# Kernel optimization log

Hardware: AMD Instinct MI355X
Metric: run time of the kernel (lower is better)

The kernel has to match this reference:

```python
import jax, jax.numpy as jnp
import numpy as np

B, S, H = 4, 2048, 1024

def setup_inputs() -> dict:
    key = jax.random.key(0)
    ks = jax.random.split(key, 4)
    scale = 1.0 / np.sqrt(H)
    x = jax.random.normal(ks[0], (B, S, H), dtype=jnp.float32)
    Wq = jax.random.normal(ks[1], (H, H), dtype=jnp.float32) * scale
    Wk = jax.random.normal(ks[2], (H, H), dtype=jnp.float32) * scale
    Wv = jax.random.normal(ks[3], (H, H), dtype=jnp.float32) * scale
    bq = jnp.zeros((H,), dtype=jnp.float32)
    bk = jnp.zeros((H,), dtype=jnp.float32)
    bv = jnp.zeros((H,), dtype=jnp.float32)
    return {"x": x, "Wq": Wq, "bq": bq, "Wk": Wk, "bk": bk, "Wv": Wv, "bv": bv}

def reference(x, Wq, bq, Wk, bk, Wv, bv):
    # Linear: y = x @ W^T + b (torch nn.Linear convention)
    Q = jnp.einsum('bsh,oh->bso', x, Wq) + bq
    K = jnp.einsum('bsh,oh->bso', x, Wk) + bk
    V = jnp.einsum('bsh,oh->bso', x, Wv) + bv
    scores = jnp.einsum('bqh,bkh->bqk', Q, K) / jnp.sqrt(jnp.float32(H))
    attn = jax.nn.softmax(scores, axis=-1)
    return jnp.einsum('bqk,bkh->bqh', attn, V)
```

## Files before the change

kernel.cpp:

```cpp
#include <hip/hip_runtime.h>
#include <cstdint>
#include <cstddef>


typedef __bf16 bf16;
typedef _Float16 f16;
typedef __bf16 bf16x8 __attribute__((ext_vector_type(8)));
typedef __bf16 bf16x4 __attribute__((ext_vector_type(4)));
typedef _Float16 f16x8 __attribute__((ext_vector_type(8)));
typedef float f32x4 __attribute__((ext_vector_type(4)));

#define BM 256
#define BN 256
#define BKT 64
#define LDS_TOTAL 131072

#define XQ (8388608 / 4)
#define WQ (1048576 / 4)
__global__ __launch_bounds__(256)
void cvt_all(const float* __restrict__ x, const float* __restrict__ Wq,
             const float* __restrict__ Wk, const float* __restrict__ Wv,
             bf16* __restrict__ xb, bf16* __restrict__ Wqkv)
{
    const int i = blockIdx.x * 256 + threadIdx.x;
    const float* src;
    bf16* dst;
    if (i < XQ) {
        src = x + 4 * (size_t)i;
        dst = xb + 4 * (size_t)i;
    } else {
        const int j = i - XQ;
        const int w = j / WQ;
        const int off = j - w * WQ;
        const float* ws_ = (w == 0) ? Wq : (w == 1) ? Wk : Wv;
        src = ws_ + 4 * (size_t)off;
        dst = Wqkv + 4 * (size_t)j;
    }
    f32x4 v = *(const f32x4*)src;
    bf16x4 o;
#pragma unroll
    for (int r = 0; r < 4; ++r) o[r] = (bf16)v[r];
    *(bf16x4*)dst = o;
}

template <int OUTMODE>
__global__ __launch_bounds__(512, 2)
void gemm256(const bf16* __restrict__ A, const bf16* __restrict__ Bm,
             const float* __restrict__ bias0, const float* __restrict__ bias1,
             const float* __restrict__ bias2, void* __restrict__ C,
             int K, int N, float alpha, long zA, long zB, long zC)
{
    extern __shared__ __align__(16) char smem[];
    auto lds3 = (__attribute__((address_space(3))) char*)smem;

    const int tid  = threadIdx.x;
    const int lane = tid & 63;
    const int wid  = tid >> 6;
    const int quad = lane >> 4;
    const int l16  = lane & 15;
    const int wr   = (wid >> 2) * 128;
    const int wc   = (wid & 3) * 64;

    const int m0 = blockIdx.y * BM;
    const int n0 = blockIdx.x * BN;
    const int z  = blockIdx.z;

    const bf16* Ab = A + (size_t)z * zA + (size_t)m0 * K;
    const bf16* Bb = Bm + (size_t)z * zB + (size_t)n0 * K;

    const int sr  = tid >> 3;
    const int sc  = (tid & 7) ^ (sr & 7);
    const size_t soff = (size_t)sr * K + (size_t)sc * 8;
    const long  hstep = 64L * K;
    const long  h1off = 128L * K;
    const unsigned dmabase = (unsigned)(wid * 1024);

#define STAGE(g, ldsoff)                                                       \
    do {                                                                       \
        __builtin_amdgcn_global_load_lds(                                      \
            (const __attribute__((address_space(1))) void*)((g) + soff),       \
            (__attribute__((address_space(3))) void*)(lds3 + (ldsoff) + dmabase), \
            16, 0, 0);                                                         \
        __builtin_amdgcn_global_load_lds(                                      \
            (const __attribute__((address_space(1))) void*)((g) + soff + hstep), \
            (__attribute__((address_space(3))) void*)(lds3 + (ldsoff) + 8192 + dmabase), \
            16, 0, 0);                                                         \
    } while (0)

    const char* pa = (const char*)smem + (wid >> 2) * 16384 + l16 * 128;
    const char* pb = (const char*)smem + 65536 + ((wid & 3) >> 1) * 16384 +
                     (((wid & 3) & 1) * 64 + l16) * 128;
    const int x0 = (quad ^ (l16 & 7)) * 16;

    const int NT = K / BKT;
    f32x4 acc[8][4] = {};
    bf16x8 af[4][2], b01[2][2], b23[2][2];

    STAGE(Ab, 0u);             STAGE(Ab + h1off, 16384u);
    STAGE(Bb, 65536u);         STAGE(Bb + h1off, 65536u + 16384u);
    STAGE(Ab + 64, 32768u);    STAGE(Ab + 64 + h1off, 32768u + 16384u);
    asm volatile("s_waitcnt vmcnt(4)\n\ts_barrier" ::: "memory");

    for (int t = 0; t < NT; ++t) {
        const int d  = (t & 1) * 32768;
        const int dn = 32768 - d;
        const char* paT = pa + d;
        const char* pbT = pb + d;

#pragma unroll
        for (int i = 0; i < 4; ++i) {
            af[i][0] = *(const bf16x8*)(paT + i * 2048 + x0);
            af[i][1] = *(const bf16x8*)(paT + i * 2048 + (x0 ^ 64));
        }
#pragma unroll
        for (int j = 0; j < 2; ++j) {
            b01[j][0] = *(const bf16x8*)(pbT + j * 2048 + x0);
            b01[j][1] = *(const bf16x8*)(pbT + j * 2048 + (x0 ^ 64));
        }
        if (t + 1 < NT) STAGE(Bb + (t + 1) * 64, 65536u + dn);
        asm volatile("s_barrier\n\ts_waitcnt lgkmcnt(0)" ::: "memory");
        __builtin_amdgcn_s_setprio(1);
#pragma unroll
        for (int i = 0; i < 4; ++i)
#pragma unroll
            for (int j = 0; j < 2; ++j) {
                acc[i][j] = __builtin_amdgcn_mfma_f32_16x16x32_bf16(
                    af[i][0], b01[j][0], acc[i][j], 0, 0, 0);
                acc[i][j] = __builtin_amdgcn_mfma_f32_16x16x32_bf16(
                    af[i][1], b01[j][1], acc[i][j], 0, 0, 0);
            }
        __builtin_amdgcn_s_setprio(0);
        asm volatile("s_barrier" ::: "memory");

#pragma unroll
        for (int j = 0; j < 2; ++j) {
            b23[j][0] = *(const bf16x8*)(pbT + (2 + j) * 2048 + x0);
            b23[j][1] = *(const bf16x8*)(pbT + (2 + j) * 2048 + (x0 ^ 64));
        }
        if (t + 1 < NT) STAGE(Bb + (t + 1) * 64 + h1off, 65536u + dn + 16384u);
        asm volatile("s_barrier\n\ts_waitcnt lgkmcnt(0)" ::: "memory");
        __builtin_amdgcn_s_setprio(1);
#pragma unroll
        for (int i = 0; i < 4; ++i)
#pragma unroll
            for (int j = 0; j < 2; ++j) {
                acc[i][2 + j] = __builtin_amdgcn_mfma_f32_16x16x32_bf16(
                    af[i][0], b23[j][0], acc[i][2 + j], 0, 0, 0);
                acc[i][2 + j] = __builtin_amdgcn_mfma_f32_16x16x32_bf16(
                    af[i][1], b23[j][1], acc[i][2 + j], 0, 0, 0);
            }
        __builtin_amdgcn_s_setprio(0);
        asm volatile("s_barrier" ::: "memory");

#pragma unroll
        for (int i = 0; i < 4; ++i) {
            af[i][0] = *(const bf16x8*)(paT + (4 + i) * 2048 + x0);
            af[i][1] = *(const bf16x8*)(paT + (4 + i) * 2048 + (x0 ^ 64));
        }
        asm volatile("s_barrier\n\ts_waitcnt lgkmcnt(0)" ::: "memory");
        __builtin_amdgcn_s_setprio(1);
#pragma unroll
        for (int i = 0; i < 4; ++i)
#pragma unroll
            for (int j = 0; j < 2; ++j) {
                acc[4 + i][2 + j] = __builtin_amdgcn_mfma_f32_16x16x32_bf16(
                    af[i][0], b23[j][0], acc[4 + i][2 + j], 0, 0, 0);
                acc[4 + i][2 + j] = __builtin_amdgcn_mfma_f32_16x16x32_bf16(
                    af[i][1], b23[j][1], acc[4 + i][2 + j], 0, 0, 0);
            }
        __builtin_amdgcn_s_setprio(0);
        asm volatile("s_barrier" ::: "memory");

#pragma unroll
        for (int j = 0; j < 2; ++j) {
            b01[j][0] = *(const bf16x8*)(pbT + j * 2048 + x0);
            b01[j][1] = *(const bf16x8*)(pbT + j * 2048 + (x0 ^ 64));
        }
        if (t + 2 < NT) {
            STAGE(Ab + (t + 2) * 64, (unsigned)d);
            STAGE(Ab + (t + 2) * 64 + h1off, (unsigned)d + 16384u);
        }
        asm volatile("s_barrier\n\ts_waitcnt lgkmcnt(0)" ::: "memory");
        __builtin_amdgcn_s_setprio(1);
#pragma unroll
        for (int i = 0; i < 4; ++i)
#pragma unroll
            for (int j = 0; j < 2; ++j) {
                acc[4 + i][j] = __builtin_amdgcn_mfma_f32_16x16x32_bf16(
                    af[i][0], b01[j][0], acc[4 + i][j], 0, 0, 0);
                acc[4 + i][j] = __builtin_amdgcn_mfma_f32_16x16x32_bf16(
                    af[i][1], b01[j][1], acc[4 + i][j], 0, 0, 0);
            }
        __builtin_amdgcn_s_setprio(0);
        if (t + 2 < NT)
            asm volatile("s_waitcnt vmcnt(4)\n\ts_barrier" ::: "memory");
        else if (t + 1 < NT)
            asm volatile("s_waitcnt vmcnt(0)\n\ts_barrier" ::: "memory");
    }
#undef STAGE

#pragma unroll
    for (int j = 0; j < 4; ++j) {
        const int col3 = n0 + wc + j * 16 + l16;
#pragma unroll
        for (int i = 0; i < 8; ++i) {
            const int rbase = m0 + wr + i * 16 + quad * 4;
            if (OUTMODE == 2) {
                f16* Cf = (f16*)C + (size_t)z * zC;
#pragma unroll
                for (int r = 0; r < 4; ++r)
                    Cf[(size_t)(rbase + r) * N + col3] = (f16)(acc[i][j][r] * alpha);
            } else if (OUTMODE == 3) {
                float* Cf = (float*)C + (size_t)z * zC;
#pragma unroll
                for (int r = 0; r < 4; ++r)
                    Cf[(size_t)(rbase + r) * N + col3] = acc[i][j][r];
            } else {
                const int mat = col3 >> 10;
                const int col = col3 & 1023;
                const float* bp = (mat == 0) ? bias0 : (mat == 1) ? bias1 : bias2;
                const float bj = bp[col];
                if (mat < 2) {
                    bf16* Cb = (bf16*)C + (size_t)mat * (8u << 20);
#pragma unroll
                    for (int r = 0; r < 4; ++r)
                        Cb[(size_t)(rbase + r) * 1024 + col] =
                            (bf16)(acc[i][j][r] + bj);
                } else {
                    bf16* Cb = (bf16*)C + (size_t)(16u << 20);
                    const int b = rbase >> 11;
                    const int s = rbase & 2047;
                    bf16x4 tmp;
#pragma unroll
                    for (int r = 0; r < 4; ++r) tmp[r] = (bf16)(acc[i][j][r] + bj);
                    *(bf16x4*)(Cb + (((size_t)((b << 10) + col)) << 11) + s) = tmp;
                }
            }
        }
    }
}

__device__ __forceinline__ float wred_max(float v)
{
#pragma unroll
    for (int o = 32; o > 0; o >>= 1) v = fmaxf(v, __shfl_xor(v, o, 64));
    return v;
}
__device__ __forceinline__ float wred_sum(float v)
{
#pragma unroll
    for (int o = 32; o > 0; o >>= 1) v += __shfl_xor(v, o, 64);
    return v;
}

__global__ __launch_bounds__(256)
void softmax_rows(const f16* __restrict__ Sc, bf16* __restrict__ P)
{
    constexpr int NC = 2048;
    const size_t row = blockIdx.x;
    const f16* src = Sc + row * NC;
    bf16* dst = P + row * NC;
    const int tid = threadIdx.x;

    f16x8 in = *(const f16x8*)(src + tid * 8);
    float v[8];
    float m = -3.4e38f;
#pragma unroll
    for (int i = 0; i < 8; ++i) {
        v[i] = (float)in[i];
        m = fmaxf(m, v[i]);
    }
    m = wred_max(m);

    __shared__ float redm[4], reds[4];
    if ((tid & 63) == 0) redm[tid >> 6] = m;
    __syncthreads();
    m = fmaxf(fmaxf(redm[0], redm[1]), fmaxf(redm[2], redm[3]));

    float s = 0.f;
#pragma unroll
    for (int i = 0; i < 8; ++i) { v[i] = __expf(v[i] - m); s += v[i]; }
    s = wred_sum(s);
    if ((tid & 63) == 0) reds[tid >> 6] = s;
    __syncthreads();
    s = reds[0] + reds[1] + reds[2] + reds[3];

    const float inv = 1.f / s;
    bf16x8 o;
#pragma unroll
    for (int i = 0; i < 8; ++i) o[i] = (bf16)(v[i] * inv);
    *(bf16x8*)(dst + tid * 8) = o;
}

extern "C" void kernel_launch(void* const* d_in, const int* in_sizes, int n_in,
                              void* d_out, int out_size, void* d_ws, size_t ws_size,
                              hipStream_t stream)
{
    constexpr int B = 4, S = 2048, H = 1024;
    const float* x  = (const float*)d_in[0];
    const float* Wq = (const float*)d_in[1];
    const float* bq = (const float*)d_in[2];
    const float* Wk = (const float*)d_in[3];
    const float* bk = (const float*)d_in[4];
    const float* Wv = (const float*)d_in[5];
    const float* bv = (const float*)d_in[6];
    float* out = (float*)d_out;

    char* ws = (char*)d_ws;
    bf16* xb   = (bf16*)ws;
    bf16* Wqkv = (bf16*)(ws + (size_t)(16 << 20));
    bf16* Q    = (bf16*)(ws + (size_t)(22 << 20));
    bf16* Kp   = (bf16*)(ws + (size_t)(38 << 20));
    bf16* Vt   = (bf16*)(ws + (size_t)(54 << 20));
    f16*  Sc   = (f16*) (ws + (size_t)(70 << 20));
    bf16* P    = (bf16*)(ws + (size_t)(22 << 20));

    static bool attr_done = false;
    if (!attr_done) {
        attr_done = true;
        (void)hipFuncSetAttribute(reinterpret_cast<const void*>(gemm256<4>),
                                  hipFuncAttributeMaxDynamicSharedMemorySize,
                                  LDS_TOTAL);
        (void)hipFuncSetAttribute(reinterpret_cast<const void*>(gemm256<2>),
                                  hipFuncAttributeMaxDynamicSharedMemorySize,
                                  LDS_TOTAL);
        (void)hipFuncSetAttribute(reinterpret_cast<const void*>(gemm256<3>),
                                  hipFuncAttributeMaxDynamicSharedMemorySize,
                                  LDS_TOTAL);
    }

    dim3 blk(256, 1, 1);
    dim3 blk512(512, 1, 1);

    cvt_all<<<dim3((XQ + 3 * WQ) / 256), blk, 0, stream>>>(
        x, Wq, Wk, Wv, xb, Wqkv);

    gemm256<4><<<dim3(3 * H / BN, (B * S) / BM, 1), blk512, LDS_TOTAL, stream>>>(
        xb, Wqkv, bq, bk, bv, Q, H, 3 * H, 1.0f, 0, 0, 0);

    gemm256<2><<<dim3(S / BN, S / BM, B), blk512, LDS_TOTAL, stream>>>(
        Q, Kp, nullptr, nullptr, nullptr, Sc, H, S, 0.03125f,
        (long)S * H, (long)S * H, (long)S * S);

    softmax_rows<<<dim3(B * S), blk, 0, stream>>>(Sc, P);

    gemm256<3><<<dim3(H / BN, S / BM, B), blk512, LDS_TOTAL, stream>>>(
        P, Vt, nullptr, nullptr, nullptr, out, S, H, 1.0f,
        (long)S * S, (long)H * S, (long)S * H);
}
```

Measured before the change: 288.8 us.

## Add 256x128 GEMM tile variant, XCD block swizzle, and fewer barriers

Templates the GEMM on the number of N-waves so the P·V GEMM uses 256x128 tiles, doubling its grid from 128 to 256 blocks to fill more CUs, with a triple-buffered A ring and double-buffered B. Remaps block IDs with a chunked interleave across 8 XCDs so neighbouring tiles share L2. It also removes most intra-iteration barrier and lgkmcnt waits in the 256x256 path, relying on the compiler's waits for LDS reads. This risks LDS hazards if the remaining synchronization is insufficient, and the swizzle assumes the block count divides by 8.

```diff
diff --git a/kernel.cpp b/kernel.cpp
--- a/kernel.cpp
+++ b/kernel.cpp
@@ -11,7 +11,6 @@
 typedef float f32x4 __attribute__((ext_vector_type(4)));
 
 #define BM 256
-#define BN 256
 #define BKT 64
 #define LDS_TOTAL 131072
 
@@ -43,13 +42,14 @@
     *(bf16x4*)dst = o;
 }
 
-template <int OUTMODE>
+template <int OUTMODE, int NW_N>
 __global__ __launch_bounds__(512, 2)
 void gemm256(const bf16* __restrict__ A, const bf16* __restrict__ Bm,
              const float* __restrict__ bias0, const float* __restrict__ bias1,
              const float* __restrict__ bias2, void* __restrict__ C,
              int K, int N, float alpha, long zA, long zB, long zC)
 {
+    constexpr int MI = 2 * NW_N;
     extern __shared__ __align__(16) char smem[];
     auto lds3 = (__attribute__((address_space(3))) char*)smem;
 
@@ -58,12 +58,20 @@
     const int wid  = tid >> 6;
     const int quad = lane >> 4;
     const int l16  = lane & 15;
-    const int wr   = (wid >> 2) * 128;
-    const int wc   = (wid & 3) * 64;
-
-    const int m0 = blockIdx.y * BM;
-    const int n0 = blockIdx.x * BN;
-    const int z  = blockIdx.z;
+    const int wc   = (wid % NW_N) * 64;
+    const int wr   = (wid / NW_N) * (MI * 16);
+
+    const unsigned gx = gridDim.x, gy = gridDim.y;
+    unsigned flat = blockIdx.x + gx * (blockIdx.y + gy * blockIdx.z);
+    const unsigned chunk = (gx * gy * gridDim.z) >> 3;
+    flat = (flat & 7u) * chunk + (flat >> 3);
+    const int bx = flat % gx;
+    const unsigned r2 = flat / gx;
+    const int by = r2 % gy;
+    const int z  = r2 / gy;
+
+    const int m0 = by * BM;
+    const int n0 = bx * (NW_N * 64);
 
     const bf16* Ab = A + (size_t)z * zA + (size_t)m0 * K;
     const bf16* Bb = Bm + (size_t)z * zB + (size_t)n0 * K;
@@ -87,115 +95,177 @@
             16, 0, 0);                                                         \
     } while (0)
 
-    const char* pa = (const char*)smem + (wid >> 2) * 16384 + l16 * 128;
-    const char* pb = (const char*)smem + 65536 + ((wid & 3) >> 1) * 16384 +
-                     (((wid & 3) & 1) * 64 + l16) * 128;
+    const char* pa = (const char*)smem + (wr + l16) * 128;
     const int x0 = (quad ^ (l16 & 7)) * 16;
 
     const int NT = K / BKT;
-    f32x4 acc[8][4] = {};
-    bf16x8 af[4][2], b01[2][2], b23[2][2];
-
-    STAGE(Ab, 0u);             STAGE(Ab + h1off, 16384u);
-    STAGE(Bb, 65536u);         STAGE(Bb + h1off, 65536u + 16384u);
-    STAGE(Ab + 64, 32768u);    STAGE(Ab + 64 + h1off, 32768u + 16384u);
-    asm volatile("s_waitcnt vmcnt(4)\n\ts_barrier" ::: "memory");
-
-    for (int t = 0; t < NT; ++t) {
-        const int d  = (t & 1) * 32768;
-        const int dn = 32768 - d;
-        const char* paT = pa + d;
-        const char* pbT = pb + d;
-
-#pragma unroll
-        for (int i = 0; i < 4; ++i) {
-            af[i][0] = *(const bf16x8*)(paT + i * 2048 + x0);
-            af[i][1] = *(const bf16x8*)(paT + i * 2048 + (x0 ^ 64));
+    f32x4 acc[MI][4] = {};
+
+    if constexpr (NW_N == 4) {
+        const char* pb = (const char*)smem + 65536 + (wc + l16) * 128;
+        bf16x8 af[4][2], b01[2][2], b23[2][2];
+
+        STAGE(Ab, 0u);           STAGE(Ab + h1off, 16384u);
+        STAGE(Bb, 65536u);       STAGE(Bb + h1off, 65536u + 16384u);
+        STAGE(Ab + 64, 32768u);  STAGE(Ab + 64 + h1off, 32768u + 16384u);
+        asm volatile("s_waitcnt vmcnt(4)\n\ts_barrier" ::: "memory");
+
+        for (int t = 0; t < NT; ++t) {
+            const unsigned d  = (unsigned)(t & 1) * 32768u;
+            const unsigned dn = 32768u - d;
+            const char* paT = pa + d;
+            const char* pbT = pb + d;
+
+#pragma unroll
+            for (int i = 0; i < 4; ++i) {
+                af[i][0] = *(const bf16x8*)(paT + i * 2048 + x0);
+                af[i][1] = *(const bf16x8*)(paT + i * 2048 + (x0 ^ 64));
+            }
+#pragma unroll
+            for (int j = 0; j < 2; ++j) {
+                b01[j][0] = *(const bf16x8*)(pbT + j * 2048 + x0);
+                b01[j][1] = *(const bf16x8*)(pbT + j * 2048 + (x0 ^ 64));
+            }
+            if (t + 1 < NT) STAGE(Bb + (t + 1) * 64, 65536u + dn);
+            __builtin_amdgcn_s_setprio(1);
+#pragma unroll
+            for (int i = 0; i < 4; ++i)
+#pragma unroll
+                for (int j = 0; j < 2; ++j) {
+                    acc[i][j] = __builtin_amdgcn_mfma_f32_16x16x32_bf16(
+                        af[i][0], b01[j][0], acc[i][j], 0, 0, 0);
+                    acc[i][j] = __builtin_amdgcn_mfma_f32_16x16x32_bf16(
+                        af[i][1], b01[j][1], acc[i][j], 0, 0, 0);
+                }
+            __builtin_amdgcn_s_setprio(0);
+
+#pragma unroll
+            for (int j = 0; j < 2; ++j) {
+                b23[j][0] = *(const bf16x8*)(pbT + (2 + j) * 2048 + x0);
+                b23[j][1] = *(const bf16x8*)(pbT + (2 + j) * 2048 + (x0 ^ 64));
+            }
+            if (t + 1 < NT) STAGE(Bb + (t + 1) * 64 + h1off, 65536u + dn + 16384u);
+            __builtin_amdgcn_s_setprio(1);
+#pragma unroll
+            for (int i = 0; i < 4; ++i)
+#pragma unroll
+                for (int j = 0; j < 2; ++j) {
+                    acc[i][2 + j] = __builtin_amdgcn_mfma_f32_16x16x32_bf16(
+                        af[i][0], b23[j][0], acc[i][2 + j], 0, 0, 0);
+                    acc[i][2 + j] = __builtin_amdgcn_mfma_f32_16x16x32_bf16(
+                        af[i][1], b23[j][1], acc[i][2 + j], 0, 0, 0);
+                }
+            __builtin_amdgcn_s_setprio(0);
+
+#pragma unroll
+            for (int i = 0; i < 4; ++i) {
+                af[i][0] = *(const bf16x8*)(paT + (4 + i) * 2048 + x0);
+                af[i][1] = *(const bf16x8*)(paT + (4 + i) * 2048 + (x0 ^ 64));
+            }
+            __builtin_amdgcn_s_setprio(1);
+#pragma unroll
+            for (int i = 0; i < 4; ++i)
+#pragma unroll
+                for (int j = 0; j < 2; ++j) {
+                    acc[4 + i][2 + j] = __builtin_amdgcn_mfma_f32_16x16x32_bf16(
+                        af[i][0], b23[j][0], acc[4 + i][2 + j], 0, 0, 0);
+                    acc[4 + i][2 + j] = __builtin_amdgcn_mfma_f32_16x16x32_bf16(
+                        af[i][1], b23[j][1], acc[4 + i][2 + j], 0, 0, 0);
+                }
+            __builtin_amdgcn_s_setprio(0);
+
+            asm volatile("s_barrier" ::: "memory");
+
+#pragma unroll
+            for (int j = 0; j < 2; ++j) {
+                b01[j][0] = *(const bf16x8*)(pbT + j * 2048 + x0);
+                b01[j][1] = *(const bf16x8*)(pbT + j * 2048 + (x0 ^ 64));
+            }
+            if (t + 2 < NT) {
+                STAGE(Ab + (t + 2) * 64, d);
+                STAGE(Ab + (t + 2) * 64 + h1off, d + 16384u);
+            }
+            __builtin_amdgcn_s_setprio(1);
+#pragma unroll
+            for (int i = 0; i < 4; ++i)
+#pragma unroll
+                for (int j = 0; j < 2; ++j) {
+                    acc[4 + i][j] = __builtin_amdgcn_mfma_f32_16x16x32_bf16(
+                        af[i][0], b01[j][0], acc[4 + i][j], 0, 0, 0);
+                    acc[4 + i][j] = __builtin_amdgcn_mfma_f32_16x16x32_bf16(
+                        af[i][1], b01[j][1], acc[4 + i][j], 0, 0, 0);
+                }
+            __builtin_amdgcn_s_setprio(0);
+
+            if (t + 2 < NT)
+                asm volatile("s_waitcnt vmcnt(4)\n\ts_barrier" ::: "memory");
+            else if (t + 1 < NT)
+                asm volatile("s_waitcnt vmcnt(0)\n\ts_barrier" ::: "memory");
         }
-#pragma unroll
-        for (int j = 0; j < 2; ++j) {
-            b01[j][0] = *(const bf16x8*)(pbT + j * 2048 + x0);
-            b01[j][1] = *(const bf16x8*)(pbT + j * 2048 + (x0 ^ 64));
+    } else {
+        bf16x8 af[2][2], bfr[4][2];
+
+        STAGE(Ab, 0u);           STAGE(Ab + h1off, 16384u);
+        STAGE(Bb, 98304u);
+        STAGE(Ab + 64, 32768u);  STAGE(Ab + 64 + h1off, 32768u + 16384u);
+        asm volatile("s_waitcnt vmcnt(4)\n\ts_barrier" ::: "memory");
+
+        for (int t = 0; t < NT; ++t) {
+            const char* paT = pa + (unsigned)(t % 3) * 32768u;
+            const char* pbT = (const char*)smem + 98304u +
+                              (unsigned)(t & 1) * 16384u + (wc + l16) * 128;
+
+#pragma unroll
+            for (int i = 0; i < 2; ++i) {
+                af[i][0] = *(const bf16x8*)(paT + i * 2048 + x0);
+                af[i][1] = *(const bf16x8*)(paT + i * 2048 + (x0 ^ 64));
+            }
+#pragma unroll
+            for (int j = 0; j < 4; ++j) {
+                bfr[j][0] = *(const bf16x8*)(pbT + j * 2048 + x0);
+                bfr[j][1] = *(const bf16x8*)(pbT + j * 2048 + (x0 ^ 64));
+            }
+            if (t + 1 < NT)
+                STAGE(Bb + (t + 1) * 64, 98304u + (unsigned)((t + 1) & 1) * 16384u);
+            __builtin_amdgcn_s_setprio(1);
+#pragma unroll
+            for (int i = 0; i < 2; ++i)
+#pragma unroll
+                for (int j = 0; j < 4; ++j) {
+                    acc[i][j] = __builtin_amdgcn_mfma_f32_16x16x32_bf16(
+                        af[i][0], bfr[j][0], acc[i][j], 0, 0, 0);
+                    acc[i][j] = __builtin_amdgcn_mfma_f32_16x16x32_bf16(
+                        af[i][1], bfr[j][1], acc[i][j], 0, 0, 0);
+                }
+            __builtin_amdgcn_s_setprio(0);
+
+#pragma unroll
+            for (int i = 0; i < 2; ++i) {
+                af[i][0] = *(const bf16x8*)(paT + (2 + i) * 2048 + x0);
+                af[i][1] = *(const bf16x8*)(paT + (2 + i) * 2048 + (x0 ^ 64));
+            }
+            if (t + 2 < NT) {
+                const unsigned da = (unsigned)((t + 2) % 3) * 32768u;
+                STAGE(Ab + (t + 2) * 64, da);
+                STAGE(Ab + (t + 2) * 64 + h1off, da + 16384u);
+            }
+            __builtin_amdgcn_s_setprio(1);
+#pragma unroll
+            for (int i = 0; i < 2; ++i)
+#pragma unroll
+                for (int j = 0; j < 4; ++j) {
+                    acc[2 + i][j] = __builtin_amdgcn_mfma_f32_16x16x32_bf16(
+                        af[i][0], bfr[j][0], acc[2 + i][j], 0, 0, 0);
+                    acc[2 + i][j] = __builtin_amdgcn_mfma_f32_16x16x32_bf16(
+                        af[i][1], bfr[j][1], acc[2 + i][j], 0, 0, 0);
+                }
+            __builtin_amdgcn_s_setprio(0);
+
+            if (t + 2 < NT)
+                asm volatile("s_waitcnt vmcnt(4)\n\ts_barrier" ::: "memory");
+            else if (t + 1 < NT)
+                asm volatile("s_waitcnt vmcnt(0)\n\ts_barrier" ::: "memory");
         }
-        if (t + 1 < NT) STAGE(Bb + (t + 1) * 64, 65536u + dn);
-        asm volatile("s_barrier\n\ts_waitcnt lgkmcnt(0)" ::: "memory");
-        __builtin_amdgcn_s_setprio(1);
-#pragma unroll
-        for (int i = 0; i < 4; ++i)
-#pragma unroll
-            for (int j = 0; j < 2; ++j) {
-                acc[i][j] = __builtin_amdgcn_mfma_f32_16x16x32_bf16(
-                    af[i][0], b01[j][0], acc[i][j], 0, 0, 0);
-                acc[i][j] = __builtin_amdgcn_mfma_f32_16x16x32_bf16(
-                    af[i][1], b01[j][1], acc[i][j], 0, 0, 0);
-            }
-        __builtin_amdgcn_s_setprio(0);
-        asm volatile("s_barrier" ::: "memory");
-
-#pragma unroll
-        for (int j = 0; j < 2; ++j) {
-            b23[j][0] = *(const bf16x8*)(pbT + (2 + j) * 2048 + x0);
-            b23[j][1] = *(const bf16x8*)(pbT + (2 + j) * 2048 + (x0 ^ 64));
-        }
-        if (t + 1 < NT) STAGE(Bb + (t + 1) * 64 + h1off, 65536u + dn + 16384u);
-        asm volatile("s_barrier\n\ts_waitcnt lgkmcnt(0)" ::: "memory");
-        __builtin_amdgcn_s_setprio(1);
-#pragma unroll
-        for (int i = 0; i < 4; ++i)
-#pragma unroll
-            for (int j = 0; j < 2; ++j) {
-                acc[i][2 + j] = __builtin_amdgcn_mfma_f32_16x16x32_bf16(
-                    af[i][0], b23[j][0], acc[i][2 + j], 0, 0, 0);
-                acc[i][2 + j] = __builtin_amdgcn_mfma_f32_16x16x32_bf16(
-                    af[i][1], b23[j][1], acc[i][2 + j], 0, 0, 0);
-            }
-        __builtin_amdgcn_s_setprio(0);
-        asm volatile("s_barrier" ::: "memory");
-
-#pragma unroll
-        for (int i = 0; i < 4; ++i) {
-            af[i][0] = *(const bf16x8*)(paT + (4 + i) * 2048 + x0);
-            af[i][1] = *(const bf16x8*)(paT + (4 + i) * 2048 + (x0 ^ 64));
-        }
-        asm volatile("s_barrier\n\ts_waitcnt lgkmcnt(0)" ::: "memory");
-        __builtin_amdgcn_s_setprio(1);
-#pragma unroll
-        for (int i = 0; i < 4; ++i)
-#pragma unroll
-            for (int j = 0; j < 2; ++j) {
-                acc[4 + i][2 + j] = __builtin_amdgcn_mfma_f32_16x16x32_bf16(
-                    af[i][0], b23[j][0], acc[4 + i][2 + j], 0, 0, 0);
-                acc[4 + i][2 + j] = __builtin_amdgcn_mfma_f32_16x16x32_bf16(
-                    af[i][1], b23[j][1], acc[4 + i][2 + j], 0, 0, 0);
-            }
-        __builtin_amdgcn_s_setprio(0);
-        asm volatile("s_barrier" ::: "memory");
-
-#pragma unroll
-        for (int j = 0; j < 2; ++j) {
-            b01[j][0] = *(const bf16x8*)(pbT + j * 2048 + x0);
-            b01[j][1] = *(const bf16x8*)(pbT + j * 2048 + (x0 ^ 64));
-        }
-        if (t + 2 < NT) {
-            STAGE(Ab + (t + 2) * 64, (unsigned)d);
-            STAGE(Ab + (t + 2) * 64 + h1off, (unsigned)d + 16384u);
-        }
-        asm volatile("s_barrier\n\ts_waitcnt lgkmcnt(0)" ::: "memory");
-        __builtin_amdgcn_s_setprio(1);
-#pragma unroll
-        for (int i = 0; i < 4; ++i)
-#pragma unroll
-            for (int j = 0; j < 2; ++j) {
-                acc[4 + i][j] = __builtin_amdgcn_mfma_f32_16x16x32_bf16(
-                    af[i][0], b01[j][0], acc[4 + i][j], 0, 0, 0);
-                acc[4 + i][j] = __builtin_amdgcn_mfma_f32_16x16x32_bf16(
-                    af[i][1], b01[j][1], acc[4 + i][j], 0, 0, 0);
-            }
-        __builtin_amdgcn_s_setprio(0);
-        if (t + 2 < NT)
-            asm volatile("s_waitcnt vmcnt(4)\n\ts_barrier" ::: "memory");
-        else if (t + 1 < NT)
-            asm volatile("s_waitcnt vmcnt(0)\n\ts_barrier" ::: "memory");
     }
 #undef STAGE
 
@@ -203,7 +273,7 @@
     for (int j = 0; j < 4; ++j) {
         const int col3 = n0 + wc + j * 16 + l16;
 #pragma unroll
-        for (int i = 0; i < 8; ++i) {
+        for (int i = 0; i < MI; ++i) {
             const int rbase = m0 + wr + i * 16 + quad * 4;
             if (OUTMODE == 2) {
                 f16* Cf = (f16*)C + (size_t)z * zC;
@@ -318,13 +388,13 @@
     static bool attr_done = false;
     if (!attr_done) {
         attr_done = true;
-        (void)hipFuncSetAttribute(reinterpret_cast<const void*>(gemm256<4>),
+        (void)hipFuncSetAttribute(reinterpret_cast<const void*>(gemm256<4, 4>),
                                   hipFuncAttributeMaxDynamicSharedMemorySize,
                                   LDS_TOTAL);
-        (void)hipFuncSetAttribute(reinterpret_cast<const void*>(gemm256<2>),
+        (void)hipFuncSetAttribute(reinterpret_cast<const void*>(gemm256<2, 4>),
                                   hipFuncAttributeMaxDynamicSharedMemorySize,
                                   LDS_TOTAL);
-        (void)hipFuncSetAttribute(reinterpret_cast<const void*>(gemm256<3>),
+        (void)hipFuncSetAttribute(reinterpret_cast<const void*>(gemm256<3, 2>),
                                   hipFuncAttributeMaxDynamicSharedMemorySize,
                                   LDS_TOTAL);
     }
@@ -335,16 +405,16 @@
     cvt_all<<<dim3((XQ + 3 * WQ) / 256), blk, 0, stream>>>(
         x, Wq, Wk, Wv, xb, Wqkv);
 
-    gemm256<4><<<dim3(3 * H / BN, (B * S) / BM, 1), blk512, LDS_TOTAL, stream>>>(
+    gemm256<4, 4><<<dim3(3 * H / 256, (B * S) / BM, 1), blk512, LDS_TOTAL, stream>>>(
         xb, Wqkv, bq, bk, bv, Q, H, 3 * H, 1.0f, 0, 0, 0);
 
-    gemm256<2><<<dim3(S / BN, S / BM, B), blk512, LDS_TOTAL, stream>>>(
+    gemm256<2, 4><<<dim3(S / 256, S / BM, B), blk512, LDS_TOTAL, stream>>>(
         Q, Kp, nullptr, nullptr, nullptr, Sc, H, S, 0.03125f,
         (long)S * H, (long)S * H, (long)S * S);
 
     softmax_rows<<<dim3(B * S), blk, 0, stream>>>(Sc, P);
 
-    gemm256<3><<<dim3(H / BN, S / BM, B), blk512, LDS_TOTAL, stream>>>(
+    gemm256<3, 2><<<dim3(H / 128, S / BM, B), blk512, LDS_TOTAL, stream>>>(
         P, Vt, nullptr, nullptr, nullptr, out, S, H, 1.0f,
         (long)S * S, (long)H * S, (long)S * H);
 }
```

Measured after the change: 248.5 us. 13.9% less time.
